# Optimization experiments

Hardware: AMD Instinct MI355X
Metric: run time of the kernel (lower is better)

The kernel has to match this reference:

```python
import jax, jax.numpy as jnp
import numpy as np

TOP_P = 0.9
B, D, H, O, E = 8192, 1024, 2048, 1024, 8


def setup_inputs() -> dict:
    key = jax.random.key(0)
    ks = jax.random.split(key, 6)
    def init(k, shape, fan_in):
        return (jax.random.normal(k, shape, jnp.float32) * (fan_in ** -0.5)).astype(jnp.float32)
    return {
        "x": jax.random.normal(ks[0], (B, D), jnp.float32),
        "gate_w": init(ks[1], (D, E), D),
        "gate_b": jnp.zeros((E,), jnp.float32),
        "w1": init(ks[2], (E, D, H), D),
        "b1": jnp.zeros((E, H), jnp.float32),
        "w2": init(ks[3], (E, H, O), H),
        "b2": jnp.zeros((E, O), jnp.float32),
    }


def reference(x, gate_w, gate_b, w1, b1, w2, b2):
    # gate + softmax
    logits = x @ gate_w + gate_b                      # [B,E]
    probs = jax.nn.softmax(logits, axis=-1)
    # all-expert MLP (batched over experts); torch GELU default is exact (erf)
    h = jax.nn.gelu(jnp.einsum('bd,edh->beh', x, w1) + b1[None], approximate=False)
    all_out = jnp.einsum('beh,eho->beo', h, w2) + b2[None]  # [B,E,O]
    # routing (entropy) loss
    routing_loss = (-jnp.sum(probs * jnp.log(probs + 1e-8), axis=-1)).mean()
    # diversity (gram logdet) loss
    mean_probs = probs.mean(axis=0)[:, None]          # [E,1]
    expert_mean = all_out.mean(axis=0)                # [E,O]
    norm = jnp.linalg.norm(expert_mean, axis=1, keepdims=True) + 1e-6
    V = mean_probs * (expert_mean / norm)             # [E,O]
    gram = V @ V.T + 1e-6 * jnp.eye(E, dtype=V.dtype)
    diversity_loss = -jnp.linalg.slogdet(gram)[1]
    # top-p mask over experts
    order = jnp.argsort(-probs, axis=-1)              # descending
    p_sorted = jnp.take_along_axis(probs, order, axis=-1)
    cum = jnp.cumsum(p_sorted, axis=-1)
    mask = cum <= TOP_P
    mask = mask.at[:, 0].set(True)
    inv = jnp.argsort(order, axis=-1)                 # inverse permutation
    mask_orig = jnp.take_along_axis(mask, inv, axis=-1)
    # normalized masked combine
    mp = probs * mask_orig.astype(probs.dtype)
    wts = mp / (mp.sum(axis=-1, keepdims=True) + 1e-8)
    output = jnp.einsum('be,beo->bo', wts, all_out)
    return output, routing_loss, diversity_loss
```

## Files before the change

### kernel.cpp

```cpp
#include <hip/hip_runtime.h>
#include <cstdint>
#include <cstddef>
#include <cmath>

#define B_ 8192
#define D_ 1024
#define H_ 2048
#define O_ 1024
#define E_ 8

typedef __bf16 bf16;
typedef __bf16 bf16x8 __attribute__((ext_vector_type(8)));
typedef __bf16 bf16x4v __attribute__((ext_vector_type(4)));
typedef float f32x4 __attribute__((ext_vector_type(4)));

typedef __attribute__((address_space(1))) void gvoid;
typedef __attribute__((address_space(3))) void lvoid;

__device__ __forceinline__ void gload16(const void* g, void* l) {
  __builtin_amdgcn_global_load_lds((gvoid*)g, (lvoid*)l, 16u, 0, 0);
}

__device__ __forceinline__ float fast_erff(float x) {
  float ax = __builtin_fabsf(x);
  float t = 1.f / (1.f + 0.3275911f * ax);
  float p = t * (0.254829592f +
            t * (-0.284496736f +
            t * (1.421413741f +
            t * (-1.453152027f +
            t * 1.061405429f))));
  float r = 1.f - p * __expf(-ax * ax);
  return __builtin_copysignf(r, x);
}
__device__ __forceinline__ float gelu_exact(float v) {
  return 0.5f * v * (1.f + fast_erff(v * 0.70710678118654752f));
}

__global__ __launch_bounds__(256) void convert_x_kernel(const float* __restrict__ x,
                                                        bf16* __restrict__ xb) {
  size_t i = (size_t)blockIdx.x * 256 + threadIdx.x;
  float4 v = ((const float4*)x)[i];
  bf16x4v o;
  o[0] = (bf16)v.x; o[1] = (bf16)v.y; o[2] = (bf16)v.z; o[3] = (bf16)v.w;
  ((bf16x4v*)xb)[i] = o;
}

__global__ __launch_bounds__(256) void transpose_w_kernel(const float* __restrict__ w,
                                                          bf16* __restrict__ wt,
                                                          int R, int C) {
  __shared__ float tile[32][33];
  int e = blockIdx.z;
  int c0 = blockIdx.x * 32, r0 = blockIdx.y * 32;
  int tx = threadIdx.x, ty = threadIdx.y;
  const float* we = w + (size_t)e * R * C;
  bf16* wte = wt + (size_t)e * R * C;
#pragma unroll
  for (int k = 0; k < 4; ++k) {
    int r = ty + 8 * k;
    tile[r][tx] = we[(size_t)(r0 + r) * C + c0 + tx];
  }
  __syncthreads();
#pragma unroll
  for (int k = 0; k < 4; ++k) {
    int c = ty + 8 * k;
    wte[(size_t)(c0 + c) * R + r0 + tx] = (bf16)tile[tx][c];
  }
}

__global__ __launch_bounds__(256) void gating_kernel(const float* __restrict__ x,
                                                     const float* __restrict__ gw,
                                                     const float* __restrict__ gb,
                                                     float* __restrict__ probs,
                                                     float* __restrict__ wts,
                                                     float* __restrict__ ent) {
  int w = threadIdx.x >> 6, l = threadIdx.x & 63;
  int b = blockIdx.x * 4 + w;
  const float* xr = x + (size_t)b * D_;
  float acc[E_];
#pragma unroll
  for (int e = 0; e < E_; ++e) acc[e] = 0.f;
  for (int j = 0; j < D_ / 64; ++j) {
    int d = j * 64 + l;
    float xv = xr[d];
    const float* g = gw + (size_t)d * E_;
#pragma unroll
    for (int e = 0; e < E_; ++e) acc[e] += xv * g[e];
  }
#pragma unroll
  for (int off = 32; off; off >>= 1)
#pragma unroll
    for (int e = 0; e < E_; ++e) acc[e] += __shfl_down(acc[e], off);

  if (l == 0) {
    float lg[E_], p[E_];
    float mx = -1e30f;
#pragma unroll
    for (int e = 0; e < E_; ++e) { lg[e] = acc[e] + gb[e]; mx = fmaxf(mx, lg[e]); }
    float s = 0.f;
#pragma unroll
    for (int e = 0; e < E_; ++e) { p[e] = expf(lg[e] - mx); s += p[e]; }
    float inv = 1.f / s;
    float en = 0.f;
#pragma unroll
    for (int e = 0; e < E_; ++e) { p[e] *= inv; en -= p[e] * logf(p[e] + 1e-8f); }
    ent[b] = en;
#pragma unroll
    for (int e = 0; e < E_; ++e) probs[(size_t)b * E_ + e] = p[e];
    int idx[E_]; float ps[E_];
#pragma unroll
    for (int e = 0; e < E_; ++e) { idx[e] = e; ps[e] = p[e]; }
    for (int i = 0; i < E_ - 1; ++i)
      for (int j = 0; j < E_ - 1 - i; ++j)
        if (ps[j] < ps[j + 1]) {
          float tp = ps[j]; ps[j] = ps[j + 1]; ps[j + 1] = tp;
          int ti = idx[j]; idx[j] = idx[j + 1]; idx[j + 1] = ti;
        }
    float cum = 0.f; float mp[E_];
#pragma unroll
    for (int e = 0; e < E_; ++e) mp[e] = 0.f;
    for (int i = 0; i < E_; ++i) {
      cum += ps[i];
      bool m = (cum <= 0.9f) || (i == 0);
      if (m) mp[idx[i]] = ps[i];
    }
    float ssum = 0.f;
#pragma unroll
    for (int e = 0; e < E_; ++e) ssum += mp[e];
    float invs = 1.f / (ssum + 1e-8f);
#pragma unroll
    for (int e = 0; e < E_; ++e) wts[(size_t)b * E_ + e] = mp[e] * invs;
  }
}


__device__ __forceinline__ void stage_half(const bf16* __restrict__ src, int ld,
                                           int kOff, bf16* ldsHalf,
                                           int w, int row16, int posG) {
#pragma unroll
  for (int c2 = 0; c2 < 2; ++c2) {
    const int call = w * 2 + c2;
    const int r = call * 16 + row16;
    const int gchunk = posG ^ ((r >> 1) & 3);
    gload16(src + (size_t)r * ld + kOff + gchunk * 8, ldsHalf + call * 512);
  }
}

__device__ __forceinline__ void phase_pre_mfma() {
  __builtin_amdgcn_s_barrier();
  asm volatile("s_waitcnt lgkmcnt(0)" ::: "memory");
  __builtin_amdgcn_sched_barrier(0);
  __builtin_amdgcn_s_setprio(1);
}
__device__ __forceinline__ void phase_post_mfma() {
  __builtin_amdgcn_s_setprio(0);
  __builtin_amdgcn_s_barrier();
}

#define MFMA_QUAD(MB)                                                                   \
  _Pragma("unroll") for (int m_ = 0; m_ < 4; ++m_)                                      \
  _Pragma("unroll") for (int n_ = 0; n_ < 4; ++n_)                                      \
    acc[(MB) + m_][n_] =                                                                \
        __builtin_amdgcn_mfma_f32_16x16x32_bf16(afr[m_], bfr[n_], acc[(MB) + m_][n_], 0, 0, 0);

__global__ __launch_bounds__(512) void gemm1_v6_kernel(const bf16* __restrict__ xb,
                                                       const bf16* __restrict__ w1t,
                                                       const float* __restrict__ b1,
                                                       const float* __restrict__ wts,
                                                       bf16* __restrict__ h_chunk,
                                                       float* __restrict__ hsum,
                                                       int rowOffset, int Bc, int nRow) {
  __shared__ bf16 smem[65536];
  const int tid = threadIdx.x;
  const int w = tid >> 6, l = tid & 63;
  const int wm = w >> 2, wn = w & 3;
  const int fm = l & 15, fc = l >> 4;
  const int posOff = (fc ^ ((fm >> 1) & 3)) * 8;
  const int row16 = l >> 2, posG = l & 3;

  const int flat = blockIdx.x;
  const int xcd = flat & 7, lin = flat >> 3;
  const int cb = xcd * 8 + lin / nRow;
  const int rb = lin % nRow;
  const int colBase = cb * 256;
  const int rowGlobal = rowOffset + rb * 256;
  const int e = colBase >> 11;

  f32x4 acc[8][4];
#pragma unroll
  for (int m = 0; m < 8; ++m)
#pragma unroll
    for (int n = 0; n < 4; ++n) acc[m][n] = 0.f;

  const bf16* Ag = xb + (size_t)rowGlobal * D_;
  const bf16* Bg = w1t + (size_t)colBase * D_;

  stage_half(Ag, D_, 0,  smem,          w, row16, posG);
  stage_half(Bg, D_, 0,  smem + 16384,  w, row16, posG);
  stage_half(Ag, D_, 32, smem + 8192,   w, row16, posG);
  stage_half(Bg, D_, 32, smem + 24576,  w, row16, posG);
  stage_half(Ag, D_, 64, smem + 32768,  w, row16, posG);
  stage_half(Bg, D_, 64, smem + 49152,  w, row16, posG);
  asm volatile("s_waitcnt vmcnt(4)" ::: "memory");
  __builtin_amdgcn_s_barrier();

  const int nt = D_ / 64;
  bf16x8 afr[4], bfr[4];
#pragma unroll 2
  for (int t = 0; t < nt; ++t) {
    const int p = t & 1;
    bf16* bufA = smem + p * 32768;
    bf16* bufB = bufA + 16384;
    bf16* nbufA = smem + (p ^ 1) * 32768;
    bf16* nbufB = nbufA + 16384;
    const bf16* laneA = bufA + (size_t)(wm * 128 + fm) * 32 + posOff;
    const bf16* laneB = bufB + (size_t)(wn * 64 + fm) * 32 + posOff;

#pragma unroll
    for (int n = 0; n < 4; ++n) bfr[n] = *(const bf16x8*)(laneB + n * 512);
#pragma unroll
    for (int m = 0; m < 4; ++m) afr[m] = *(const bf16x8*)(laneA + m * 512);
    if (t + 1 < nt) stage_half(Ag, D_, (t + 1) * 64 + 32, nbufA + 8192, w, row16, posG);
    phase_pre_mfma();
    MFMA_QUAD(0)
    phase_post_mfma();

#pragma unroll
    for (int m = 0; m < 4; ++m) afr[m] = *(const bf16x8*)(laneA + 2048 + m * 512);
    if (t + 1 < nt) stage_half(Bg, D_, (t + 1) * 64 + 32, nbufB + 8192, w, row16, posG);
    phase_pre_mfma();
    MFMA_QUAD(4)
    phase_post_mfma();

#pragma unroll
    for (int n = 0; n < 4; ++n) bfr[n] = *(const bf16x8*)(laneB + 8192 + n * 512);
#pragma unroll
    for (int m = 0; m < 4; ++m) afr[m] = *(const bf16x8*)(laneA + 8192 + m * 512);
    if (t + 2 < nt) stage_half(Ag, D_, (t + 2) * 64, bufA, w, row16, posG);
    phase_pre_mfma();
    MFMA_QUAD(0)
    phase_post_mfma();

#pragma unroll
    for (int m = 0; m < 4; ++m) afr[m] = *(const bf16x8*)(laneA + 10240 + m * 512);
    if (t + 2 < nt) stage_half(Bg, D_, (t + 2) * 64, bufB, w, row16, posG);
    __builtin_amdgcn_s_barrier();
    asm volatile("s_waitcnt lgkmcnt(0)" ::: "memory");
    __builtin_amdgcn_sched_barrier(0);
    __builtin_amdgcn_s_setprio(1);
    MFMA_QUAD(4)
    __builtin_amdgcn_s_setprio(0);
    if (t < nt - 2) asm volatile("s_waitcnt vmcnt(4)" ::: "memory");
    else            asm volatile("s_waitcnt vmcnt(0)" ::: "memory");
    __builtin_amdgcn_s_barrier();
  }

  __syncthreads();
  float wgt[8][4];
#pragma unroll
  for (int m = 0; m < 8; ++m)
#pragma unroll
    for (int i = 0; i < 4; ++i)
      wgt[m][i] = wts[(size_t)(rowGlobal + wm * 128 + m * 16 + fc * 4 + i) * E_ + e];

  bf16* he = h_chunk + (size_t)e * Bc * H_;
  const int hc0 = colBase & (H_ - 1);
  const int rowLocal = rb * 256;

#pragma unroll
  for (int hh = 0; hh < 2; ++hh) {
    if (wm == hh) {
#pragma unroll
      for (int n = 0; n < 4; ++n) {
        const int col = wn * 64 + n * 16 + fm;
        const float bias = b1[colBase + col];
        float csum = 0.f;
#pragma unroll
        for (int m = 0; m < 8; ++m) {
          const int rbse = m * 16 + fc * 4;
#pragma unroll
          for (int i = 0; i < 4; ++i) {
            float v = gelu_exact(acc[m][n][i] + bias);
            csum += v;
            smem[(size_t)(rbse + i) * 264 + col] = (bf16)(v * wgt[m][i]);
          }
        }
        csum += __shfl_down(csum, 32);
        csum += __shfl_down(csum, 16);
        if (fc == 0) atomicAdd(&hsum[colBase + col], csum);
      }
    }
    __syncthreads();
#pragma unroll
    for (int j = 0; j < 8; ++j) {
      const int u = j * 512 + tid;
      const int row = u >> 5, ch = u & 31;
      bf16x8 v = *(const bf16x8*)(smem + (size_t)row * 264 + ch * 8);
      *(bf16x8*)(he + (size_t)(rowLocal + hh * 128 + row) * H_ + hc0 + ch * 8) = v;
    }
    __syncthreads();
  }
}

template <int SPLIT>
__global__ __launch_bounds__(512) void gemm2_v6_kernel(const bf16* __restrict__ h_chunk,
                                                       const bf16* __restrict__ w2t,
                                                       const float* __restrict__ b2,
                                                       const float* __restrict__ wts,
                                                       float* __restrict__ out_chunk,
                                                       int rowOffset, int Bc, int nRow) {
  __shared__ bf16 smem[65536];
  const int tid = threadIdx.x;
  const int w = tid >> 6, l = tid & 63;
  const int wm = w >> 2, wn = w & 3;
  const int fm = l & 15, fc = l >> 4;
  const int posOff = (fc ^ ((fm >> 1) & 3)) * 8;
  const int row16 = l >> 2, posG = l & 3;

  const int flat = blockIdx.x;
  const int xcd = flat & 7, lin = flat >> 3;
  const int cb = xcd >> 1;
  const int rb = (xcd & 1) * (nRow >> 1) + lin;
  const int colBase = cb * 256;
  const int rowLocal = rb * 256;
  const int s = blockIdx.y;
  constexpr int g = E_ / SPLIT;
  const int e0 = s * g;
  constexpr int nt = g * (H_ / 64);

  f32x4 acc[8][4];
#pragma unroll
  for (int m = 0; m < 8; ++m)
#pragma unroll
    for (int n = 0; n < 4; ++n) acc[m][n] = 0.f;

  const bf16* hA = h_chunk + (size_t)rowLocal * H_;
  const bf16* wB = w2t + (size_t)colBase * H_;
  const size_t strideA = (size_t)Bc * H_;
  const size_t strideB = (size_t)O_ * H_;
  auto srcA = [&](int tt) { return hA + (size_t)(e0 + (tt >> 5)) * strideA; };
  auto srcB = [&](int tt) { return wB + (size_t)(e0 + (tt >> 5)) * strideB; };
  auto koff = [&](int tt) { return (tt & 31) * 64; };

  stage_half(srcA(0), H_, koff(0),      smem,          w, row16, posG);
  stage_half(srcB(0), H_, koff(0),      smem + 16384,  w, row16, posG);
  stage_half(srcA(0), H_, koff(0) + 32, smem + 8192,   w, row16, posG);
  stage_half(srcB(0), H_, koff(0) + 32, smem + 24576,  w, row16, posG);
  stage_half(srcA(1), H_, koff(1),      smem + 32768,  w, row16, posG);
  stage_half(srcB(1), H_, koff(1),      smem + 49152,  w, row16, posG);
  asm volatile("s_waitcnt vmcnt(4)" ::: "memory");
  __builtin_amdgcn_s_barrier();

  bf16x8 afr[4], bfr[4];
#pragma unroll 2
  for (int t = 0; t < nt; ++t) {
    const int p = t & 1;
    bf16* bufA = smem + p * 32768;
    bf16* bufB = bufA + 16384;
    bf16* nbufA = smem + (p ^ 1) * 32768;
    bf16* nbufB = nbufA + 16384;
    const bf16* laneA = bufA + (size_t)(wm * 128 + fm) * 32 + posOff;
    const bf16* laneB = bufB + (size_t)(wn * 64 + fm) * 32 + posOff;

#pragma unroll
    for (int n = 0; n < 4; ++n) bfr[n] = *(const bf16x8*)(laneB + n * 512);
#pragma unroll
    for (int m = 0; m < 4; ++m) afr[m] = *(const bf16x8*)(laneA + m * 512);
    if (t + 1 < nt) stage_half(srcA(t + 1), H_, koff(t + 1) + 32, nbufA + 8192, w, row16, posG);
    phase_pre_mfma();
    MFMA_QUAD(0)
    phase_post_mfma();

#pragma unroll
    for (int m = 0; m < 4; ++m) afr[m] = *(const bf16x8*)(laneA + 2048 + m * 512);
    if (t + 1 < nt) stage_half(srcB(t + 1), H_, koff(t + 1) + 32, nbufB + 8192, w, row16, posG);
    phase_pre_mfma();
    MFMA_QUAD(4)
    phase_post_mfma();

#pragma unroll
    for (int n = 0; n < 4; ++n) bfr[n] = *(const bf16x8*)(laneB + 8192 + n * 512);
#pragma unroll
    for (int m = 0; m < 4; ++m) afr[m] = *(const bf16x8*)(laneA + 8192 + m * 512);
    if (t + 2 < nt) stage_half(srcA(t + 2), H_, koff(t + 2), bufA, w, row16, posG);
    phase_pre_mfma();
    MFMA_QUAD(0)
    phase_post_mfma();

#pragma unroll
    for (int m = 0; m < 4; ++m) afr[m] = *(const bf16x8*)(laneA + 10240 + m * 512);
    if (t + 2 < nt) stage_half(srcB(t + 2), H_, koff(t + 2), bufB, w, row16, posG);
    __builtin_amdgcn_s_barrier();
    asm volatile("s_waitcnt lgkmcnt(0)" ::: "memory");
    __builtin_amdgcn_sched_barrier(0);
    __builtin_amdgcn_s_setprio(1);
    MFMA_QUAD(4)
    __builtin_amdgcn_s_setprio(0);
    if (t < nt - 2) asm volatile("s_waitcnt vmcnt(4)" ::: "memory");
    else            asm volatile("s_waitcnt vmcnt(0)" ::: "memory");
    __builtin_amdgcn_s_barrier();
  }

#pragma unroll
  for (int n = 0; n < 4; ++n) {
    const int gc = colBase + wn * 64 + n * 16 + fm;
    float b2v[E_];
    if (s == 0) {
#pragma unroll
      for (int ee = 0; ee < E_; ++ee) b2v[ee] = b2[(size_t)ee * O_ + gc];
    }
#pragma unroll
    for (int m = 0; m < 8; ++m) {
      const int lrb = rowLocal + wm * 128 + m * 16 + fc * 4;
#pragma unroll
      for (int i = 0; i < 4; ++i) {
        const int lr2 = lrb + i;
        float v = acc[m][n][i];
        if (s == 0) {
          const float4* wr = (const float4*)(wts + (size_t)(rowOffset + lr2) * E_);
          float4 w0 = wr[0], w1v = wr[1];
          v += w0.x * b2v[0] + w0.y * b2v[1] + w0.z * b2v[2] + w0.w * b2v[3] +
               w1v.x * b2v[4] + w1v.y * b2v[5] + w1v.z * b2v[6] + w1v.w * b2v[7];
        }
        float* op = out_chunk + (size_t)lr2 * O_ + gc;
        if (SPLIT == 1) *op = v;
        else atomicAdd(op, v);
      }
    }
  }
}

__device__ __forceinline__ void gemm_loop(const bf16* __restrict__ A,
                                          const bf16* __restrict__ Bt,
                                          int K, int rowBase, int colBase,
                                          bf16* lA, bf16* lB, f32x4 acc[4][4]) {
  const int tid = threadIdx.x;
  const int w = tid >> 6, l = tid & 63;
  const int wm = w >> 1, wn = w & 1;
  const int fm = l & 15, fc = l >> 4;
  const int lr = l >> 2, lc = l & 3;
  const int sr0 = (w * 2 + 0) * 16 + lr;
  const int sr1 = (w * 2 + 1) * 16 + lr;
  const int cg0 = lc ^ ((sr0 >> 1) & 3);
  const int cg1 = lc ^ ((sr1 >> 1) & 3);
  const bf16* gA0 = A + (size_t)(rowBase + sr0) * K + cg0 * 8;
  const bf16* gA1 = A + (size_t)(rowBase + sr1) * K + cg1 * 8;
  const bf16* gB0 = Bt + (size_t)(colBase + sr0) * K + cg0 * 8;
  const bf16* gB1 = Bt + (size_t)(colBase + sr1) * K + cg1 * 8;
  bf16* lA0 = lA + (w * 2 + 0) * 512;
  bf16* lA1 = lA + (w * 2 + 1) * 512;
  bf16* lB0 = lB + (w * 2 + 0) * 512;
  bf16* lB1 = lB + (w * 2 + 1) * 512;

  for (int k0 = 0; k0 < K; k0 += 32) {
    __syncthreads();
    gload16(gA0 + k0, lA0);
    gload16(gA1 + k0, lA1);
    gload16(gB0 + k0, lB0);
    gload16(gB1 + k0, lB1);
    __syncthreads();

    bf16x8 af[4], bb[4];
#pragma unroll
    for (int mt = 0; mt < 4; ++mt) {
      int r = wm * 64 + mt * 16 + fm;
      af[mt] = *(const bf16x8*)(lA + (size_t)(r * 4 + (fc ^ ((r >> 1) & 3))) * 8);
    }
#pragma unroll
    for (int nt = 0; nt < 4; ++nt) {
      int r = wn * 64 + nt * 16 + fm;
      bb[nt] = *(const bf16x8*)(lB + (size_t)(r * 4 + (fc ^ ((r >> 1) & 3))) * 8);
    }
#pragma unroll
    for (int mt = 0; mt < 4; ++mt)
#pragma unroll
      for (int nt = 0; nt < 4; ++nt)
        acc[mt][nt] = __builtin_amdgcn_mfma_f32_16x16x32_bf16(af[mt], bb[nt], acc[mt][nt], 0, 0, 0);
  }
}

__global__ __launch_bounds__(256) void gemm1_gelu_kernel(const bf16* __restrict__ xb,
                                                         const bf16* __restrict__ w1te,
                                                         const float* __restrict__ b1e,
                                                         bf16* __restrict__ h) {
  __shared__ bf16 lA[128 * 32];
  __shared__ bf16 lB[128 * 32];
  f32x4 acc[4][4];
#pragma unroll
  for (int mt = 0; mt < 4; ++mt)
#pragma unroll
    for (int nt = 0; nt < 4; ++nt) acc[mt][nt] = 0.f;

  int rowBase = blockIdx.y * 128, colBase = blockIdx.x * 128;
  gemm_loop(xb, w1te, D_, rowBase, colBase, lA, lB, acc);

  const int w = threadIdx.x >> 6, l = threadIdx.x & 63;
  const int wm = w >> 1, wn = w & 1;
#pragma unroll
  for (int mt = 0; mt < 4; ++mt)
#pragma unroll
    for (int nt = 0; nt < 4; ++nt) {
      int gc = colBase + wn * 64 + nt * 16 + (l & 15);
      float bias = b1e[gc];
#pragma unroll
      for (int i = 0; i < 4; ++i) {
        int gr = rowBase + wm * 64 + mt * 16 + (l >> 4) * 4 + i;
        float v = gelu_exact(acc[mt][nt][i] + bias);
        h[(size_t)gr * H_ + gc] = (bf16)v;
      }
    }
}

__global__ __launch_bounds__(256) void gemm2_fused_kernel(const bf16* __restrict__ h,
                                                          const bf16* __restrict__ w2te,
                                                          const float* __restrict__ b2e,
                                                          const float* __restrict__ wts,
                                                          int e,
                                                          float* __restrict__ out,
                                                          float* __restrict__ esum) {
  __shared__ bf16 lA[128 * 32];
  __shared__ bf16 lB[128 * 32];
  f32x4 acc[4][4];
#pragma unroll
  for (int mt = 0; mt < 4; ++mt)
#pragma unroll
    for (int nt = 0; nt < 4; ++nt) acc[mt][nt] = 0.f;

  int rowBase = blockIdx.y * 128, colBase = blockIdx.x * 128;
  gemm_loop(h, w2te, H_, rowBase, colBase, lA, lB, acc);

  const int w = threadIdx.x >> 6, l = threadIdx.x & 63;
  const int wm = w >> 1, wn = w & 1;
#pragma unroll
  for (int nt = 0; nt < 4; ++nt) {
    int gc = colBase + wn * 64 + nt * 16 + (l & 15);
    float bias = b2e[gc];
    float csum = 0.f;
#pragma unroll
    for (int mt = 0; mt < 4; ++mt) {
      int grb = rowBase + wm * 64 + mt * 16 + (l >> 4) * 4;
#pragma unroll
      for (int i = 0; i < 4; ++i) {
        int gr = grb + i;
        float v = acc[mt][nt][i] + bias;
        csum += v;
        float wgt = wts[(size_t)gr * E_ + e];
        float* op = out + (size_t)gr * O_ + gc;
        *op += wgt * v;
      }
    }
    csum += __shfl_down(csum, 32);
    csum += __shfl_down(csum, 16);
    if ((l >> 4) == 0) atomicAdd(&esum[(size_t)e * O_ + gc], csum);
  }
}

template <int MODE>
__global__ __launch_bounds__(256) void scalars_kernel(const float* __restrict__ probs,
                                                      const float* __restrict__ ent,
                                                      const float* __restrict__ esum,
                                                      const float* __restrict__ b2,
                                                      float* __restrict__ outs) {
  __shared__ float red[256];
  __shared__ float Vsh[E_][O_ + 8];
  __shared__ float mp_sh[E_], norm_sh[E_];
  __shared__ float gram[E_][E_];
  int t = threadIdx.x;

  float s = 0.f;
  for (int i = t; i < B_; i += 256) s += ent[i];
  red[t] = s; __syncthreads();
  for (int off = 128; off; off >>= 1) { if (t < off) red[t] += red[t + off]; __syncthreads(); }
  if (t == 0) outs[0] = red[0] / (float)B_;
  __syncthreads();

  float mp[E_];
#pragma unroll
  for (int e = 0; e < E_; ++e) mp[e] = 0.f;
  for (int i = t; i < B_; i += 256) {
#pragma unroll
    for (int e = 0; e < E_; ++e) mp[e] += probs[(size_t)i * E_ + e];
  }
  for (int e = 0; e < E_; ++e) {
    red[t] = mp[e]; __syncthreads();
    for (int off = 128; off; off >>= 1) { if (t < off) red[t] += red[t + off]; __syncthreads(); }
    if (t == 0) mp_sh[e] = red[0] / (float)B_;
    __syncthreads();
  }

  for (int e = 0; e < E_; ++e) {
    float ss = 0.f;
    for (int o = t; o < O_; o += 256) {
      float m = esum[(size_t)e * O_ + o] / (float)B_;
      if (MODE == 1) m += b2[(size_t)e * O_ + o];
      ss += m * m;
    }
    red[t] = ss; __syncthreads();
    for (int off = 128; off; off >>= 1) { if (t < off) red[t] += red[t + off]; __syncthreads(); }
    if (t == 0) norm_sh[e] = sqrtf(red[0]) + 1e-6f;
    __syncthreads();
  }

  for (int e = 0; e < E_; ++e)
    for (int o = t; o < O_; o += 256) {
      float m = esum[(size_t)e * O_ + o] / (float)B_;
      if (MODE == 1) m += b2[(size_t)e * O_ + o];
      Vsh[e][o] = mp_sh[e] * m / norm_sh[e];
    }
  __syncthreads();

  if (t < 64) {
    int i = t >> 3, j = t & 7;
    float g = 0.f;
    for (int o = 0; o < O_; ++o) g += Vsh[i][o] * Vsh[j][o];
    if (i == j) g += 1e-6f;
    gram[i][j] = g;
  }
  __syncthreads();

  if (t == 0) {
    double a[E_][E_];
    for (int i = 0; i < E_; ++i) for (int j = 0; j < E_; ++j) a[i][j] = (double)gram[i][j];
    double ld = 0.0;
    for (int k = 0; k < E_; ++k) {
      int p = k; double mx = fabs(a[k][k]);
      for (int i = k + 1; i < E_; ++i) if (fabs(a[i][k]) > mx) { mx = fabs(a[i][k]); p = i; }
      if (p != k) for (int j = 0; j < E_; ++j) { double tmp = a[k][j]; a[k][j] = a[p][j]; a[p][j] = tmp; }
      ld += log(fabs(a[k][k]));
      double inv = 1.0 / a[k][k];
      for (int i = k + 1; i < E_; ++i) {
        double f = a[i][k] * inv;
        for (int j = k; j < E_; ++j) a[i][j] -= f * a[k][j];
      }
    }
    outs[1] = (float)(-ld);
  }
}

__global__ __launch_bounds__(256) void esum_kernel(const float* __restrict__ hsum,
                                                   const float* __restrict__ w2,
                                                   float* __restrict__ esum2) {
  int e = blockIdx.y;
  int o = blockIdx.x * 256 + threadIdx.x;
  const float* w2e = w2 + (size_t)e * H_ * O_;
  const float* hs = hsum + (size_t)e * H_;
  float a0 = 0.f, a1 = 0.f;
  for (int h = 0; h < H_; h += 2) {
    a0 += hs[h] * w2e[(size_t)h * O_ + o];
    a1 += hs[h + 1] * w2e[(size_t)(h + 1) * O_ + o];
  }
  esum2[(size_t)e * O_ + o] = a0 + a1;
}

extern "C" void kernel_launch(void* const* d_in, const int* in_sizes, int n_in,
                              void* d_out, int out_size, void* d_ws, size_t ws_size,
                              hipStream_t stream) {
  const float* x  = (const float*)d_in[0];
  const float* gw = (const float*)d_in[1];
  const float* gb = (const float*)d_in[2];
  const float* w1 = (const float*)d_in[3];
  const float* b1 = (const float*)d_in[4];
  const float* w2 = (const float*)d_in[5];
  const float* b2 = (const float*)d_in[6];
  float* out = (float*)d_out;

  char* ws = (char*)d_ws;
  size_t need = 0;
  bf16* xb    = (bf16*)(ws + need); need += (size_t)B_ * D_ * 2;
  bf16* w1t   = (bf16*)(ws + need); need += (size_t)E_ * D_ * H_ * 2;
  bf16* w2t   = (bf16*)(ws + need); need += (size_t)E_ * H_ * O_ * 2;
  float* wts  = (float*)(ws + need); need += (size_t)B_ * E_ * 4;
  float* probs= (float*)(ws + need); need += (size_t)B_ * E_ * 4;
  float* ent  = (float*)(ws + need); need += (size_t)B_ * 4;
  float* hsum = (float*)(ws + need); need += (size_t)E_ * H_ * 4;
  float* esum = (float*)(ws + need); need += (size_t)E_ * O_ * 4;
  size_t need_common = need;
  bf16* h_chunk = (bf16*)(ws + need);

  int NC = 0;
  for (int nc = 1; nc <= 8; nc <<= 1) {
    size_t tot = need_common + (size_t)E_ * (B_ / nc) * H_ * 2;
    if (ws_size >= tot) { NC = nc; break; }
  }

  convert_x_kernel<<<(B_ * D_ / 4) / 256, 256, 0, stream>>>(x, xb);
  transpose_w_kernel<<<dim3(H_ / 32, D_ / 32, E_), dim3(32, 8), 0, stream>>>(w1, w1t, D_, H_);
  transpose_w_kernel<<<dim3(O_ / 32, H_ / 32, E_), dim3(32, 8), 0, stream>>>(w2, w2t, H_, O_);
  gating_kernel<<<B_ / 4, 256, 0, stream>>>(x, gw, gb, probs, wts, ent);

  if (NC > 0) {
    const int Bc = B_ / NC;
    const int nRow = Bc / 256;
    const int SPLIT = (NC == 1) ? 2 : (NC == 2) ? 4 : 8;
    hipMemsetAsync(hsum, 0, (size_t)E_ * H_ * sizeof(float), stream);
    hipMemsetAsync(out, 0, (size_t)B_ * O_ * sizeof(float), stream);
    for (int c = 0; c < NC; ++c) {
      int rowOffset = c * Bc;
      gemm1_v6_kernel<<<64 * nRow, 512, 0, stream>>>(
          xb, w1t, b1, wts, h_chunk, hsum, rowOffset, Bc, nRow);
      float* out_chunk = out + (size_t)rowOffset * O_;
      dim3 g2(4 * nRow, SPLIT);
      switch (SPLIT) {
        case 2: gemm2_v6_kernel<2><<<g2, 512, 0, stream>>>(h_chunk, w2t, b2, wts, out_chunk, rowOffset, Bc, nRow); break;
        case 4: gemm2_v6_kernel<4><<<g2, 512, 0, stream>>>(h_chunk, w2t, b2, wts, out_chunk, rowOffset, Bc, nRow); break;
        case 8: gemm2_v6_kernel<8><<<g2, 512, 0, stream>>>(h_chunk, w2t, b2, wts, out_chunk, rowOffset, Bc, nRow); break;
      }
    }
    esum_kernel<<<dim3(O_ / 256, E_), 256, 0, stream>>>(hsum, w2, esum);
    scalars_kernel<1><<<1, 256, 0, stream>>>(probs, ent, esum, b2, out + (size_t)B_ * O_);
  } else {
    bf16* he = (bf16*)(ws + need_common);
    if (ws_size < need_common + (size_t)B_ * H_ * 2) return;
    hipMemsetAsync(out, 0, (size_t)B_ * O_ * sizeof(float), stream);
    hipMemsetAsync(esum, 0, (size_t)E_ * O_ * sizeof(float), stream);
    for (int e = 0; e < E_; ++e) {
      gemm1_gelu_kernel<<<dim3(H_ / 128, B_ / 128), 256, 0, stream>>>(
          xb, w1t + (size_t)e * H_ * D_, b1 + (size_t)e * H_, he);
      gemm2_fused_kernel<<<dim3(O_ / 128, B_ / 128), 256, 0, stream>>>(
          he, w2t + (size_t)e * O_ * H_, b2 + (size_t)e * O_, wts, e, out, esum);
    }
    scalars_kernel<0><<<1, 256, 0, stream>>>(probs, ent, esum, b2, out + (size_t)B_ * O_);
  }
}
```

Before: 1.166 ms.

## Restructure GEMM main loop into two barrier phases with split LDS waits

Both GEMM kernels now share a common main-loop core that runs two phases per k-tile instead of four. The A and B global-to-LDS staging for each half-tile is issued together, and the A fragments are loaded into two register sets so the first 16 MFMAs can start after a partial lgkmcnt wait. This halves the number of workgroup barriers per iteration and overlaps LDS reads with MFMA issue, aiming to cut synchronization stalls. In exchange it uses more VGPRs for the extra fragment set, and the placement of the B staging relative to the barriers changes the hazard ordering.

```diff
diff --git a/kernel.cpp b/kernel.cpp
--- a/kernel.cpp
+++ b/kernel.cpp
@@ -145,24 +145,90 @@
   }
 }
 
-__device__ __forceinline__ void phase_pre_mfma() {
-  __builtin_amdgcn_s_barrier();
-  asm volatile("s_waitcnt lgkmcnt(0)" ::: "memory");
-  __builtin_amdgcn_sched_barrier(0);
-  __builtin_amdgcn_s_setprio(1);
-}
-__device__ __forceinline__ void phase_post_mfma() {
-  __builtin_amdgcn_s_setprio(0);
-  __builtin_amdgcn_s_barrier();
-}
-
-#define MFMA_QUAD(MB)                                                                   \
+#define MFMA16(AF, MB)                                                                  \
   _Pragma("unroll") for (int m_ = 0; m_ < 4; ++m_)                                      \
   _Pragma("unroll") for (int n_ = 0; n_ < 4; ++n_)                                      \
     acc[(MB) + m_][n_] =                                                                \
-        __builtin_amdgcn_mfma_f32_16x16x32_bf16(afr[m_], bfr[n_], acc[(MB) + m_][n_], 0, 0, 0);
-
-__global__ __launch_bounds__(512) void gemm1_v6_kernel(const bf16* __restrict__ xb,
+        __builtin_amdgcn_mfma_f32_16x16x32_bf16(AF[m_], bfr[n_], acc[(MB) + m_][n_], 0, 0, 0);
+
+template <class SA, class SB>
+__device__ __forceinline__ void gemm_core_v7(const int nt, bf16* smem,
+                                             SA srcA, SB srcB, int ldA, int ldB,
+                                             f32x4 (&acc)[8][4]) {
+  const int tid = threadIdx.x;
+  const int w = tid >> 6, l = tid & 63;
+  const int wm = w >> 2, wn = w & 3;
+  const int fm = l & 15, fc = l >> 4;
+  const int posOff = (fc ^ ((fm >> 1) & 3)) * 8;
+  const int row16 = l >> 2, posG = l & 3;
+
+  stage_half(srcA(0), ldA, 0,  smem,          w, row16, posG);
+  stage_half(srcB(0), ldB, 0,  smem + 16384,  w, row16, posG);
+  stage_half(srcA(0), ldA, 32, smem + 8192,   w, row16, posG);
+  stage_half(srcB(0), ldB, 32, smem + 24576,  w, row16, posG);
+  stage_half(srcA(1), ldA, 0,  smem + 32768,  w, row16, posG);
+  stage_half(srcB(1), ldB, 0,  smem + 49152,  w, row16, posG);
+  asm volatile("s_waitcnt vmcnt(4)" ::: "memory");
+  __builtin_amdgcn_s_barrier();
+
+  bf16x8 bfr[4], afr0[4], afr1[4];
+#pragma unroll 2
+  for (int t = 0; t < nt; ++t) {
+    const int p = t & 1;
+    bf16* bufA = smem + p * 32768;
+    bf16* bufB = bufA + 16384;
+    bf16* nbufA = smem + (p ^ 1) * 32768;
+    bf16* nbufB = nbufA + 16384;
+    const bf16* laneA = bufA + (size_t)(wm * 128 + fm) * 32 + posOff;
+    const bf16* laneB = bufB + (size_t)(wn * 64 + fm) * 32 + posOff;
+
+    if (t + 1 < nt) {
+      stage_half(srcA(t + 1), ldA, 32, nbufA + 8192, w, row16, posG);
+      stage_half(srcB(t + 1), ldB, 32, nbufB + 8192, w, row16, posG);
+    }
+#pragma unroll
+    for (int n = 0; n < 4; ++n) bfr[n] = *(const bf16x8*)(laneB + n * 512);
+#pragma unroll
+    for (int m = 0; m < 4; ++m) afr0[m] = *(const bf16x8*)(laneA + m * 512);
+    __builtin_amdgcn_sched_barrier(0);
+#pragma unroll
+    for (int m = 0; m < 4; ++m) afr1[m] = *(const bf16x8*)(laneA + 2048 + m * 512);
+    asm volatile("s_waitcnt lgkmcnt(4)" ::: "memory");
+    __builtin_amdgcn_sched_barrier(0);
+    __builtin_amdgcn_s_setprio(1);
+    MFMA16(afr0, 0)
+    asm volatile("s_waitcnt lgkmcnt(0)" ::: "memory");
+    __builtin_amdgcn_sched_barrier(0);
+    MFMA16(afr1, 4)
+    __builtin_amdgcn_s_setprio(0);
+    __builtin_amdgcn_s_barrier();
+
+    if (t + 2 < nt) {
+      stage_half(srcA(t + 2), ldA, 0, bufA, w, row16, posG);
+      stage_half(srcB(t + 2), ldB, 0, bufB, w, row16, posG);
+    }
+#pragma unroll
+    for (int n = 0; n < 4; ++n) bfr[n] = *(const bf16x8*)(laneB + 8192 + n * 512);
+#pragma unroll
+    for (int m = 0; m < 4; ++m) afr0[m] = *(const bf16x8*)(laneA + 8192 + m * 512);
+    __builtin_amdgcn_sched_barrier(0);
+#pragma unroll
+    for (int m = 0; m < 4; ++m) afr1[m] = *(const bf16x8*)(laneA + 10240 + m * 512);
+    asm volatile("s_waitcnt lgkmcnt(4)" ::: "memory");
+    __builtin_amdgcn_sched_barrier(0);
+    __builtin_amdgcn_s_setprio(1);
+    MFMA16(afr0, 0)
+    asm volatile("s_waitcnt lgkmcnt(0)" ::: "memory");
+    __builtin_amdgcn_sched_barrier(0);
+    MFMA16(afr1, 4)
+    __builtin_amdgcn_s_setprio(0);
+    if (t < nt - 2) asm volatile("s_waitcnt vmcnt(4)" ::: "memory");
+    else            asm volatile("s_waitcnt vmcnt(0)" ::: "memory");
+    __builtin_amdgcn_s_barrier();
+  }
+}
+
+__global__ __launch_bounds__(512) void gemm1_v7_kernel(const bf16* __restrict__ xb,
                                                        const bf16* __restrict__ w1t,
                                                        const float* __restrict__ b1,
                                                        const float* __restrict__ wts,
@@ -174,8 +240,6 @@
   const int w = tid >> 6, l = tid & 63;
   const int wm = w >> 2, wn = w & 3;
   const int fm = l & 15, fc = l >> 4;
-  const int posOff = (fc ^ ((fm >> 1) & 3)) * 8;
-  const int row16 = l >> 2, posG = l & 3;
 
   const int flat = blockIdx.x;
   const int xcd = flat & 7, lin = flat >> 3;
@@ -193,66 +257,10 @@
 
   const bf16* Ag = xb + (size_t)rowGlobal * D_;
   const bf16* Bg = w1t + (size_t)colBase * D_;
-
-  stage_half(Ag, D_, 0,  smem,          w, row16, posG);
-  stage_half(Bg, D_, 0,  smem + 16384,  w, row16, posG);
-  stage_half(Ag, D_, 32, smem + 8192,   w, row16, posG);
-  stage_half(Bg, D_, 32, smem + 24576,  w, row16, posG);
-  stage_half(Ag, D_, 64, smem + 32768,  w, row16, posG);
-  stage_half(Bg, D_, 64, smem + 49152,  w, row16, posG);
-  asm volatile("s_waitcnt vmcnt(4)" ::: "memory");
-  __builtin_amdgcn_s_barrier();
-
-  const int nt = D_ / 64;
-  bf16x8 afr[4], bfr[4];
-#pragma unroll 2
-  for (int t = 0; t < nt; ++t) {
-    const int p = t & 1;
-    bf16* bufA = smem + p * 32768;
-    bf16* bufB = bufA + 16384;
-    bf16* nbufA = smem + (p ^ 1) * 32768;
-    bf16* nbufB = nbufA + 16384;
-    const bf16* laneA = bufA + (size_t)(wm * 128 + fm) * 32 + posOff;
-    const bf16* laneB = bufB + (size_t)(wn * 64 + fm) * 32 + posOff;
-
-#pragma unroll
-    for (int n = 0; n < 4; ++n) bfr[n] = *(const bf16x8*)(laneB + n * 512);
-#pragma unroll
-    for (int m = 0; m < 4; ++m) afr[m] = *(const bf16x8*)(laneA + m * 512);
-    if (t + 1 < nt) stage_half(Ag, D_, (t + 1) * 64 + 32, nbufA + 8192, w, row16, posG);
-    phase_pre_mfma();
-    MFMA_QUAD(0)
-    phase_post_mfma();
-
-#pragma unroll
-    for (int m = 0; m < 4; ++m) afr[m] = *(const bf16x8*)(laneA + 2048 + m * 512);
-    if (t + 1 < nt) stage_half(Bg, D_, (t + 1) * 64 + 32, nbufB + 8192, w, row16, posG);
-    phase_pre_mfma();
-    MFMA_QUAD(4)
-    phase_post_mfma();
-
-#pragma unroll
-    for (int n = 0; n < 4; ++n) bfr[n] = *(const bf16x8*)(laneB + 8192 + n * 512);
-#pragma unroll
-    for (int m = 0; m < 4; ++m) afr[m] = *(const bf16x8*)(laneA + 8192 + m * 512);
-    if (t + 2 < nt) stage_half(Ag, D_, (t + 2) * 64, bufA, w, row16, posG);
-    phase_pre_mfma();
-    MFMA_QUAD(0)
-    phase_post_mfma();
-
-#pragma unroll
-    for (int m = 0; m < 4; ++m) afr[m] = *(const bf16x8*)(laneA + 10240 + m * 512);
-    if (t + 2 < nt) stage_half(Bg, D_, (t + 2) * 64, bufB, w, row16, posG);
-    __builtin_amdgcn_s_barrier();
-    asm volatile("s_waitcnt lgkmcnt(0)" ::: "memory");
-    __builtin_amdgcn_sched_barrier(0);
-    __builtin_amdgcn_s_setprio(1);
-    MFMA_QUAD(4)
-    __builtin_amdgcn_s_setprio(0);
-    if (t < nt - 2) asm volatile("s_waitcnt vmcnt(4)" ::: "memory");
-    else            asm volatile("s_waitcnt vmcnt(0)" ::: "memory");
-    __builtin_amdgcn_s_barrier();
-  }
+  auto srcA = [&](int tt) { return Ag + tt * 64; };
+  auto srcB = [&](int tt) { return Bg + tt * 64; };
+
+  gemm_core_v7(D_ / 64, smem, srcA, srcB, D_, D_, acc);
 
   __syncthreads();
   float wgt[8][4];
@@ -302,7 +310,7 @@
 }
 
 template <int SPLIT>
-__global__ __launch_bounds__(512) void gemm2_v6_kernel(const bf16* __restrict__ h_chunk,
+__global__ __launch_bounds__(512) void gemm2_v7_kernel(const bf16* __restrict__ h_chunk,
                                                        const bf16* __restrict__ w2t,
                                                        const float* __restrict__ b2,
                                                        const float* __restrict__ wts,
@@ -313,8 +321,6 @@
   const int w = tid >> 6, l = tid & 63;
   const int wm = w >> 2, wn = w & 3;
   const int fm = l & 15, fc = l >> 4;
-  const int posOff = (fc ^ ((fm >> 1) & 3)) * 8;
-  const int row16 = l >> 2, posG = l & 3;
 
   const int flat = blockIdx.x;
   const int xcd = flat & 7, lin = flat >> 3;
@@ -337,68 +343,10 @@
   const bf16* wB = w2t + (size_t)colBase * H_;
   const size_t strideA = (size_t)Bc * H_;
   const size_t strideB = (size_t)O_ * H_;
-  auto srcA = [&](int tt) { return hA + (size_t)(e0 + (tt >> 5)) * strideA; };
-  auto srcB = [&](int tt) { return wB + (size_t)(e0 + (tt >> 5)) * strideB; };
-  auto koff = [&](int tt) { return (tt & 31) * 64; };
-
-  stage_half(srcA(0), H_, koff(0),      smem,          w, row16, posG);
-  stage_half(srcB(0), H_, koff(0),      smem + 16384,  w, row16, posG);
-  stage_half(srcA(0), H_, koff(0) + 32, smem + 8192,   w, row16, posG);
-  stage_half(srcB(0), H_, koff(0) + 32, smem + 24576,  w, row16, posG);
-  stage_half(srcA(1), H_, koff(1),      smem + 32768,  w, row16, posG);
-  stage_half(srcB(1), H_, koff(1),      smem + 49152,  w, row16, posG);
-  asm volatile("s_waitcnt vmcnt(4)" ::: "memory");
-  __builtin_amdgcn_s_barrier();
-
-  bf16x8 afr[4], bfr[4];
-#pragma unroll 2
-  for (int t = 0; t < nt; ++t) {
-    const int p = t & 1;
-    bf16* bufA = smem + p * 32768;
-    bf16* bufB = bufA + 16384;
-    bf16* nbufA = smem + (p ^ 1) * 32768;
-    bf16* nbufB = nbufA + 16384;
-    const bf16* laneA = bufA + (size_t)(wm * 128 + fm) * 32 + posOff;
-    const bf16* laneB = bufB + (size_t)(wn * 64 + fm) * 32 + posOff;
-
-#pragma unroll
-    for (int n = 0; n < 4; ++n) bfr[n] = *(const bf16x8*)(laneB + n * 512);
-#pragma unroll
-    for (int m = 0; m < 4; ++m) afr[m] = *(const bf16x8*)(laneA + m * 512);
-    if (t + 1 < nt) stage_half(srcA(t + 1), H_, koff(t + 1) + 32, nbufA + 8192, w, row16, posG);
-    phase_pre_mfma();
-    MFMA_QUAD(0)
-    phase_post_mfma();
-
-#pragma unroll
-    for (int m = 0; m < 4; ++m) afr[m] = *(const bf16x8*)(laneA + 2048 + m * 512);
-    if (t + 1 < nt) stage_half(srcB(t + 1), H_, koff(t + 1) + 32, nbufB + 8192, w, row16, posG);
-    phase_pre_mfma();
-    MFMA_QUAD(4)
-    phase_post_mfma();
-
-#pragma unroll
-    for (int n = 0; n < 4; ++n) bfr[n] = *(const bf16x8*)(laneB + 8192 + n * 512);
-#pragma unroll
-    for (int m = 0; m < 4; ++m) afr[m] = *(const bf16x8*)(laneA + 8192 + m * 512);
-    if (t + 2 < nt) stage_half(srcA(t + 2), H_, koff(t + 2), bufA, w, row16, posG);
-    phase_pre_mfma();
-    MFMA_QUAD(0)
-    phase_post_mfma();
-
-#pragma unroll
-    for (int m = 0; m < 4; ++m) afr[m] = *(const bf16x8*)(laneA + 10240 + m * 512);
-    if (t + 2 < nt) stage_half(srcB(t + 2), H_, koff(t + 2), bufB, w, row16, posG);
-    __builtin_amdgcn_s_barrier();
-    asm volatile("s_waitcnt lgkmcnt(0)" ::: "memory");
-    __builtin_amdgcn_sched_barrier(0);
-    __builtin_amdgcn_s_setprio(1);
-    MFMA_QUAD(4)
-    __builtin_amdgcn_s_setprio(0);
-    if (t < nt - 2) asm volatile("s_waitcnt vmcnt(4)" ::: "memory");
-    else            asm volatile("s_waitcnt vmcnt(0)" ::: "memory");
-    __builtin_amdgcn_s_barrier();
-  }
+  auto srcA = [&](int tt) { return hA + (size_t)(e0 + (tt >> 5)) * strideA + (tt & 31) * 64; };
+  auto srcB = [&](int tt) { return wB + (size_t)(e0 + (tt >> 5)) * strideB + (tt & 31) * 64; };
+
+  gemm_core_v7(nt, smem, srcA, srcB, H_, H_, acc);
 
 #pragma unroll
   for (int n = 0; n < 4; ++n) {
@@ -695,14 +643,14 @@
     hipMemsetAsync(out, 0, (size_t)B_ * O_ * sizeof(float), stream);
     for (int c = 0; c < NC; ++c) {
       int rowOffset = c * Bc;
-      gemm1_v6_kernel<<<64 * nRow, 512, 0, stream>>>(
+      gemm1_v7_kernel<<<64 * nRow, 512, 0, stream>>>(
           xb, w1t, b1, wts, h_chunk, hsum, rowOffset, Bc, nRow);
       float* out_chunk = out + (size_t)rowOffset * O_;
       dim3 g2(4 * nRow, SPLIT);
       switch (SPLIT) {
-        case 2: gemm2_v6_kernel<2><<<g2, 512, 0, stream>>>(h_chunk, w2t, b2, wts, out_chunk, rowOffset, Bc, nRow); break;
-        case 4: gemm2_v6_kernel<4><<<g2, 512, 0, stream>>>(h_chunk, w2t, b2, wts, out_chunk, rowOffset, Bc, nRow); break;
-        case 8: gemm2_v6_kernel<8><<<g2, 512, 0, stream>>>(h_chunk, w2t, b2, wts, out_chunk, rowOffset, Bc, nRow); break;
+        case 2: gemm2_v7_kernel<2><<<g2, 512, 0, stream>>>(h_chunk, w2t, b2, wts, out_chunk, rowOffset, Bc, nRow); break;
+        case 4: gemm2_v7_kernel<4><<<g2, 512, 0, stream>>>(h_chunk, w2t, b2, wts, out_chunk, rowOffset, Bc, nRow); break;
+        case 8: gemm2_v7_kernel<8><<<g2, 512, 0, stream>>>(h_chunk, w2t, b2, wts, out_chunk, rowOffset, Bc, nRow); break;
       }
     }
     esum_kernel<<<dim3(O_ / 256, E_), 256, 0, stream>>>(hsum, w2, esum);
```

Result: slower. 1.323 ms (+13.5%).
